# Kernel optimization log

Measured on AMD Instinct MI355X. Metric: run time of the kernel, lower is better.

## Reference

```python
import jax, jax.numpy as jnp
import numpy as np

NEG_FILL = -10000.0  # matches masked_fill_(mask, -10000.0)


def setup_inputs() -> dict:
    key0 = jax.random.key(0)
    kq, kk, kv, km = jax.random.split(key0, 4)
    B, H, S, D = 2, 16, 2048, 64
    query = jax.random.normal(kq, (B, H, S, D), dtype=jnp.float32)
    key = jax.random.normal(kk, (B, H, S, D), dtype=jnp.float32)
    value = jax.random.normal(kv, (B, H, S, D), dtype=jnp.float32)
    # key-padding mask [B, S]; True = position is masked out
    mask = jax.random.randint(km, (B, S), 0, 2).astype(jnp.bool_)
    return {"query": query, "key": key, "value": value, "mask": mask}


def reference(query, key, value, mask):
    # scaled dot-product attention: [B,H,S,D] x [B,H,S,D] -> [B,H,S,S]
    scale = 1.0 / jnp.sqrt(jnp.asarray(query.shape[-1], query.dtype))
    scores = jnp.einsum('bhqd,bhkd->bhqk', query, key) * scale
    # mask [B,S] -> broadcast over heads and query positions as [B,1,1,S]
    scores = jnp.where(mask[:, None, None, :], jnp.asarray(NEG_FILL, scores.dtype), scores)
    attn = jax.nn.softmax(scores, axis=-1)
    # dropout probs are 0 (eval-mode identity)
    out = jnp.einsum('bhqk,bhkd->bhqd', attn, value)
    return out
```

## Files before the change

kernel.cpp:

```cpp
#include <hip/hip_runtime.h>
#include <hip/hip_bf16.h>
#include <stdint.h>

namespace {

constexpr int Bb = 2;
constexpr int Hh = 16;
constexpr int Ss = 2048;
constexpr int Dd = 64;
constexpr int KT = 64;
constexpr int NT = Ss / KT;
constexpr int TILE_BYTES = KT * Dd * 2;
constexpr int BH_BYTES = NT * TILE_BYTES;
constexpr size_t KPRE_BYTES = (size_t)Bb * Hh * Ss * Dd * 2;
constexpr size_t VPRE_OFF = KPRE_BYTES;
constexpr size_t MASK_OFF = 2 * KPRE_BYTES;
constexpr size_t WS_NEED = MASK_OFF + (size_t)Bb * NT * 8;
constexpr int NIT = 16;
constexpr int IT_BYTES = 2 * TILE_BYTES;

typedef __bf16 bf16x8 __attribute__((ext_vector_type(8)));
typedef float floatx4 __attribute__((ext_vector_type(4)));

typedef __attribute__((address_space(1))) const unsigned int guint;
typedef __attribute__((address_space(3))) unsigned int luint;

__device__ __forceinline__ void g2lds16(const void* g, void* l) {
  __builtin_amdgcn_global_load_lds((guint*)g, (luint*)l, 16, 0, 0);
}

__global__ __launch_bounds__(256) void preprocess3(
    const float* __restrict__ K, const float* __restrict__ V,
    const int* __restrict__ mask, uint8_t* __restrict__ ws)
{
  const int tid = threadIdx.x;
  const int kt = blockIdx.x;
  const int bh = blockIdx.y;

  if (blockIdx.z == 0) {
    const int c = tid & 7;
#pragma unroll
    for (int half = 0; half < 2; ++half) {
      const int row = (tid >> 3) + half * 32;
      const float4* src = (const float4*)(K + ((size_t)bh * 2048 + kt * 64 + row) * 64 + c * 8);
      const float4 a = src[0], b2 = src[1];
      bf16x8 pk;
      pk[0] = (__bf16)a.x;  pk[1] = (__bf16)a.y;  pk[2] = (__bf16)a.z;  pk[3] = (__bf16)a.w;
      pk[4] = (__bf16)b2.x; pk[5] = (__bf16)b2.y; pk[6] = (__bf16)b2.z; pk[7] = (__bf16)b2.w;
      uint8_t* dst = ws + (size_t)bh * BH_BYTES + kt * TILE_BYTES + row * 128 + ((c ^ (row & 7)) << 4);
      *(bf16x8*)dst = pk;
    }
    if (bh == 0 && kt < 16) {
      const int i = kt * 256 + tid;
      const int bb = i >> 11, key = i & 2047;
      const unsigned long long bal = __ballot(mask[bb * 2048 + key] != 0);
      if ((key & 63) == 0)
        ((unsigned long long*)(ws + MASK_OFF))[bb * NT + (key >> 6)] = bal;
    }
    return;
  }

  __shared__ float Vsh[64 * 68];
#pragma unroll
  for (int i = 0; i < 4; ++i) {
    const int vt = tid + 256 * i;
    const int row = vt >> 4, c4 = vt & 15;
    const float4 v4 = *(const float4*)(V + ((size_t)bh * 2048 + kt * 64 + row) * 64 + c4 * 4);
    *(float4*)&Vsh[row * 68 + c4 * 4] = v4;
  }
  __syncthreads();
  {
    const int c16 = tid & 7;
    const int s2 = c16 & 1, q = c16 >> 1;
    const int k0 = 32 * s2 + 4 * q;
#pragma unroll
    for (int half = 0; half < 2; ++half) {
      const int d = (tid >> 3) + half * 32;
      bf16x8 pv;
#pragma unroll
      for (int j = 0; j < 4; ++j) {
        pv[j]     = (__bf16)Vsh[(k0 + j) * 68 + d];
        pv[4 + j] = (__bf16)Vsh[(k0 + 16 + j) * 68 + d];
      }
      uint8_t* dst = ws + VPRE_OFF + (size_t)bh * BH_BYTES + kt * TILE_BYTES + d * 128 + ((c16 ^ (d & 7)) << 4);
      *(bf16x8*)dst = pv;
    }
  }
}

#define NEGM (-14426.950408889634f)
#define MFMA16 __builtin_amdgcn_mfma_f32_16x16x32_bf16

__global__ __launch_bounds__(256, 2) void attn_fused7(
    const float* __restrict__ Q, const uint8_t* __restrict__ ws,
    float* __restrict__ Out)
{
  const int tid  = threadIdx.x;
  const int wave = tid >> 6;
  const int lane = tid & 63;
  const int ln   = lane & 15;
  const int quad = lane >> 4;

  const int bh   = blockIdx.x;
  const int qblk = blockIdx.y;
  const int b    = bh >> 4;

  const float* Qb = Q + (size_t)bh * Ss * Dd;
  float*       Ob = Out + (size_t)bh * Ss * Dd;
  const uint8_t* Kpre = ws + (size_t)bh * BH_BYTES;
  const uint8_t* Vpre = ws + VPRE_OFF + (size_t)bh * BH_BYTES;
  const unsigned long long* Mbits = (const unsigned long long*)(ws + MASK_OFF) + b * NT;

  __shared__ __align__(16) __bf16 Klds[2][128 * Dd];
  __shared__ __align__(16) __bf16 Vlds[2][128 * Dd];

  const int q0A = qblk * 128 + wave * 32;
  const int q0B = q0A + 16;

  const float QS = 0.125f * 1.44269504088896340736f;
  bf16x8 aqA0, aqA1, aqB0, aqB1;
  {
    const float* qpA = Qb + (size_t)(q0A + ln) * Dd + quad * 8;
    const float* qpB = Qb + (size_t)(q0B + ln) * Dd + quad * 8;
#pragma unroll
    for (int j = 0; j < 8; ++j) {
      aqA0[j] = (__bf16)(qpA[j] * QS);
      aqA1[j] = (__bf16)(qpA[32 + j] * QS);
      aqB0[j] = (__bf16)(qpB[j] * QS);
      aqB1[j] = (__bf16)(qpB[32 + j] * QS);
    }
  }

  floatx4 oA[4], oB[4];
  floatx4 laccA = (floatx4){0.f, 0.f, 0.f, 0.f};
  floatx4 laccB = (floatx4){0.f, 0.f, 0.f, 0.f};
#pragma unroll
  for (int nd = 0; nd < 4; ++nd) {
    oA[nd] = (floatx4){0.f, 0.f, 0.f, 0.f};
    oB[nd] = (floatx4){0.f, 0.f, 0.f, 0.f};
  }

  const int swz0 = (quad ^ (ln & 7)) << 4;
  const int swz1 = ((quad + 4) ^ (ln & 7)) << 4;
  const int soff = wave * 4096 + lane * 16;

#pragma unroll
  for (int i = 0; i < 4; ++i) {
    g2lds16(Kpre + soff + i * 1024, (uint8_t*)Klds[0] + soff + i * 1024);
    g2lds16(Vpre + soff + i * 1024, (uint8_t*)Vlds[0] + soff + i * 1024);
  }

  for (int kt2 = 0; kt2 < NIT; ++kt2) {
    const int cur = kt2 & 1;
    __syncthreads();

    if (kt2 + 1 < NIT) {
      const uint8_t* kg = Kpre + (kt2 + 1) * IT_BYTES;
      const uint8_t* vg = Vpre + (kt2 + 1) * IT_BYTES;
      uint8_t* kl = (uint8_t*)Klds[cur ^ 1];
      uint8_t* vl = (uint8_t*)Vlds[cur ^ 1];
#pragma unroll
      for (int i = 0; i < 4; ++i) {
        g2lds16(kg + soff + i * 1024, kl + soff + i * 1024);
        g2lds16(vg + soff + i * 1024, vl + soff + i * 1024);
      }
    }

    const unsigned long long mb0 = Mbits[2 * kt2];
    const unsigned long long mb1 = Mbits[2 * kt2 + 1];

    const uint8_t* Kb = (const uint8_t*)Klds[cur];
    const uint8_t* Vb = (const uint8_t*)Vlds[cur];

    auto loadK = [&](int sub, bf16x8& b0, bf16x8& b1) {
      const uint8_t* krow = Kb + (sub >> 2) * 8192 + ((sub & 3) * 16 + ln) * 128;
      b0 = *(const bf16x8*)(krow + swz0);
      b1 = *(const bf16x8*)(krow + swz1);
    };
    auto loadV = [&](int p, bf16x8* w) {
      const int T = p >> 1, s2 = p & 1;
#pragma unroll
      for (int nd = 0; nd < 4; ++nd) {
        const uint8_t* vrow = Vb + T * 8192 + (nd * 16 + ln) * 128;
        w[nd] = *(const bf16x8*)(vrow + (((quad * 2 + s2) ^ (ln & 7)) << 4));
      }
    };

    __builtin_amdgcn_s_setprio(1);

    bf16x8 kf0[2][2], kf1[2][2];
    bf16x8 vf[2][4];
    loadK(0, kf0[0][0], kf1[0][0]);
    loadK(1, kf0[0][1], kf1[0][1]);
    loadV(0, vf[0]);

#pragma unroll
    for (int p = 0; p < 4; ++p) {
      const int cb = p & 1, nb = cb ^ 1;

      if (p < 3) {
        loadK(2 * p + 2, kf0[nb][0], kf1[nb][0]);
        loadK(2 * p + 3, kf0[nb][1], kf1[nb][1]);
        loadV(p + 1, vf[nb]);
      }

      const unsigned long long mbx = (p & 2) ? mb1 : mb0;
      const uint32_t bits0 = (uint32_t)(mbx >> ((((2 * p) & 3) * 16) + quad * 4));
      const uint32_t bits1 = (uint32_t)(mbx >> ((((2 * p + 1) & 3) * 16) + quad * 4));
      floatx4 sA0, sA1, sB0, sB1;
#pragma unroll
      for (int r = 0; r < 4; ++r) {
        const float b0v = ((bits0 >> r) & 1) ? NEGM : 0.f;
        const float b1v = ((bits1 >> r) & 1) ? NEGM : 0.f;
        sA0[r] = b0v; sB0[r] = b0v;
        sA1[r] = b1v; sB1[r] = b1v;
      }

      sA0 = MFMA16(kf0[cb][0], aqA0, sA0, 0, 0, 0);
      sA0 = MFMA16(kf1[cb][0], aqA1, sA0, 0, 0, 0);
      sB0 = MFMA16(kf0[cb][0], aqB0, sB0, 0, 0, 0);
      sB0 = MFMA16(kf1[cb][0], aqB1, sB0, 0, 0, 0);
      sA1 = MFMA16(kf0[cb][1], aqA0, sA1, 0, 0, 0);
      sA1 = MFMA16(kf1[cb][1], aqA1, sA1, 0, 0, 0);
      sB1 = MFMA16(kf0[cb][1], aqB0, sB1, 0, 0, 0);
      sB1 = MFMA16(kf1[cb][1], aqB1, sB1, 0, 0, 0);

      bf16x8 bpA, bpB;
#pragma unroll
      for (int r = 0; r < 4; ++r) {
        const float pA0 = __builtin_amdgcn_exp2f(sA0[r]);
        const float pA1 = __builtin_amdgcn_exp2f(sA1[r]);
        const float pB0 = __builtin_amdgcn_exp2f(sB0[r]);
        const float pB1 = __builtin_amdgcn_exp2f(sB1[r]);
        laccA[r] += pA0 + pA1;
        laccB[r] += pB0 + pB1;
        bpA[r] = (__bf16)pA0; bpA[4 + r] = (__bf16)pA1;
        bpB[r] = (__bf16)pB0; bpB[4 + r] = (__bf16)pB1;
      }

#pragma unroll
      for (int nd = 0; nd < 4; ++nd) {
        oA[nd] = MFMA16(vf[cb][nd], bpA, oA[nd], 0, 0, 0);
        oB[nd] = MFMA16(vf[cb][nd], bpB, oB[nd], 0, 0, 0);
      }
    }
    __builtin_amdgcn_s_setprio(0);
  }

  float lA = (laccA[0] + laccA[1]) + (laccA[2] + laccA[3]);
  float lB = (laccB[0] + laccB[1]) + (laccB[2] + laccB[3]);
  lA += __shfl_xor(lA, 16); lA += __shfl_xor(lA, 32);
  lB += __shfl_xor(lB, 16); lB += __shfl_xor(lB, 32);
  const float iA = 1.0f / lA, iB = 1.0f / lB;
#pragma unroll
  for (int nd = 0; nd < 4; ++nd) {
    float4 wv;
    wv.x = oA[nd][0] * iA; wv.y = oA[nd][1] * iA;
    wv.z = oA[nd][2] * iA; wv.w = oA[nd][3] * iA;
    *(float4*)(Ob + (size_t)(q0A + ln) * Dd + nd * 16 + quad * 4) = wv;
    wv.x = oB[nd][0] * iB; wv.y = oB[nd][1] * iB;
    wv.z = oB[nd][2] * iB; wv.w = oB[nd][3] * iB;
    *(float4*)(Ob + (size_t)(q0B + ln) * Dd + nd * 16 + quad * 4) = wv;
  }
}

}

extern "C" void kernel_launch(void* const* d_in, const int* in_sizes, int n_in,
                              void* d_out, int out_size, void* d_ws, size_t ws_size,
                              hipStream_t stream) {
  const float* Q   = (const float*)d_in[0];
  const float* K   = (const float*)d_in[1];
  const float* V   = (const float*)d_in[2];
  const int*  mask = (const int*)d_in[3];
  float* Out = (float*)d_out;

  preprocess3<<<dim3(32, 32, 2), 256, 0, stream>>>(K, V, mask, (uint8_t*)d_ws);
  attn_fused7<<<dim3(Bb * Hh, Ss / 128), 256, 0, stream>>>(Q, (const uint8_t*)d_ws, Out);
  (void)ws_size; (void)in_sizes; (void)n_in; (void)out_size;
}
```

Before: 135.3 us.

## Split key range across two wave groups per block with LDS reduction

Result: slower. 148.1 us (+9.4%).

```diff
diff --git a/kernel.cpp b/kernel.cpp
--- a/kernel.cpp
+++ b/kernel.cpp
@@ -16,8 +16,6 @@
 constexpr size_t VPRE_OFF = KPRE_BYTES;
 constexpr size_t MASK_OFF = 2 * KPRE_BYTES;
 constexpr size_t WS_NEED = MASK_OFF + (size_t)Bb * NT * 8;
-constexpr int NIT = 16;
-constexpr int IT_BYTES = 2 * TILE_BYTES;
 
 typedef __bf16 bf16x8 __attribute__((ext_vector_type(8)));
 typedef float floatx4 __attribute__((ext_vector_type(4)));
@@ -91,12 +89,14 @@
 #define NEGM (-14426.950408889634f)
 #define MFMA16 __builtin_amdgcn_mfma_f32_16x16x32_bf16
 
-__global__ __launch_bounds__(256, 2) void attn_fused7(
+__global__ __launch_bounds__(512, 4) void attn_fused8(
     const float* __restrict__ Q, const uint8_t* __restrict__ ws,
     float* __restrict__ Out)
 {
   const int tid  = threadIdx.x;
   const int wave = tid >> 6;
+  const int kgrp = wave >> 2;
+  const int wq   = wave & 3;
   const int lane = tid & 63;
   const int ln   = lane & 15;
   const int quad = lane >> 4;
@@ -107,14 +107,15 @@
 
   const float* Qb = Q + (size_t)bh * Ss * Dd;
   float*       Ob = Out + (size_t)bh * Ss * Dd;
-  const uint8_t* Kpre = ws + (size_t)bh * BH_BYTES;
-  const uint8_t* Vpre = ws + VPRE_OFF + (size_t)bh * BH_BYTES;
-  const unsigned long long* Mbits = (const unsigned long long*)(ws + MASK_OFF) + b * NT;
-
-  __shared__ __align__(16) __bf16 Klds[2][128 * Dd];
-  __shared__ __align__(16) __bf16 Vlds[2][128 * Dd];
-
-  const int q0A = qblk * 128 + wave * 32;
+  const uint8_t* Kpre = ws + (size_t)bh * BH_BYTES + (size_t)kgrp * 16 * TILE_BYTES;
+  const uint8_t* Vpre = ws + VPRE_OFF + (size_t)bh * BH_BYTES + (size_t)kgrp * 16 * TILE_BYTES;
+  const unsigned long long* Mbits =
+      (const unsigned long long*)(ws + MASK_OFF) + b * NT + kgrp * 16;
+
+  __shared__ __align__(16) __bf16 Klds[2][2][64 * Dd];
+  __shared__ __align__(16) __bf16 Vlds[2][2][64 * Dd];
+
+  const int q0A = qblk * 128 + wq * 32;
   const int q0B = q0A + 16;
 
   const float QS = 0.125f * 1.44269504088896340736f;
@@ -142,46 +143,44 @@
 
   const int swz0 = (quad ^ (ln & 7)) << 4;
   const int swz1 = ((quad + 4) ^ (ln & 7)) << 4;
-  const int soff = wave * 4096 + lane * 16;
-
-#pragma unroll
-  for (int i = 0; i < 4; ++i) {
-    g2lds16(Kpre + soff + i * 1024, (uint8_t*)Klds[0] + soff + i * 1024);
-    g2lds16(Vpre + soff + i * 1024, (uint8_t*)Vlds[0] + soff + i * 1024);
-  }
-
-  for (int kt2 = 0; kt2 < NIT; ++kt2) {
-    const int cur = kt2 & 1;
+  const int soff = wq * 1024 + lane * 16;
+
+#pragma unroll
+  for (int i = 0; i < 2; ++i) {
+    g2lds16(Kpre + soff + i * 4096, (uint8_t*)Klds[kgrp][0] + soff + i * 4096);
+    g2lds16(Vpre + soff + i * 4096, (uint8_t*)Vlds[kgrp][0] + soff + i * 4096);
+  }
+
+  for (int it = 0; it < 16; ++it) {
+    const int cur = it & 1;
     __syncthreads();
 
-    if (kt2 + 1 < NIT) {
-      const uint8_t* kg = Kpre + (kt2 + 1) * IT_BYTES;
-      const uint8_t* vg = Vpre + (kt2 + 1) * IT_BYTES;
-      uint8_t* kl = (uint8_t*)Klds[cur ^ 1];
-      uint8_t* vl = (uint8_t*)Vlds[cur ^ 1];
-#pragma unroll
-      for (int i = 0; i < 4; ++i) {
-        g2lds16(kg + soff + i * 1024, kl + soff + i * 1024);
-        g2lds16(vg + soff + i * 1024, vl + soff + i * 1024);
-      }
-    }
-
-    const unsigned long long mb0 = Mbits[2 * kt2];
-    const unsigned long long mb1 = Mbits[2 * kt2 + 1];
-
-    const uint8_t* Kb = (const uint8_t*)Klds[cur];
-    const uint8_t* Vb = (const uint8_t*)Vlds[cur];
+    if (it + 1 < 16) {
+      const uint8_t* kg = Kpre + (it + 1) * TILE_BYTES;
+      const uint8_t* vg = Vpre + (it + 1) * TILE_BYTES;
+      uint8_t* kl = (uint8_t*)Klds[kgrp][cur ^ 1];
+      uint8_t* vl = (uint8_t*)Vlds[kgrp][cur ^ 1];
+#pragma unroll
+      for (int i = 0; i < 2; ++i) {
+        g2lds16(kg + soff + i * 4096, kl + soff + i * 4096);
+        g2lds16(vg + soff + i * 4096, vl + soff + i * 4096);
+      }
+    }
+
+    const unsigned long long mb = Mbits[it];
+
+    const uint8_t* Kb = (const uint8_t*)Klds[kgrp][cur];
+    const uint8_t* Vb = (const uint8_t*)Vlds[kgrp][cur];
 
     auto loadK = [&](int sub, bf16x8& b0, bf16x8& b1) {
-      const uint8_t* krow = Kb + (sub >> 2) * 8192 + ((sub & 3) * 16 + ln) * 128;
+      const uint8_t* krow = Kb + (sub * 16 + ln) * 128;
       b0 = *(const bf16x8*)(krow + swz0);
       b1 = *(const bf16x8*)(krow + swz1);
     };
-    auto loadV = [&](int p, bf16x8* w) {
-      const int T = p >> 1, s2 = p & 1;
+    auto loadV = [&](int s2, bf16x8* w) {
 #pragma unroll
       for (int nd = 0; nd < 4; ++nd) {
-        const uint8_t* vrow = Vb + T * 8192 + (nd * 16 + ln) * 128;
+        const uint8_t* vrow = Vb + (nd * 16 + ln) * 128;
         w[nd] = *(const bf16x8*)(vrow + (((quad * 2 + s2) ^ (ln & 7)) << 4));
       }
     };
@@ -195,18 +194,15 @@
     loadV(0, vf[0]);
 
 #pragma unroll
-    for (int p = 0; p < 4; ++p) {
-      const int cb = p & 1, nb = cb ^ 1;
-
-      if (p < 3) {
-        loadK(2 * p + 2, kf0[nb][0], kf1[nb][0]);
-        loadK(2 * p + 3, kf0[nb][1], kf1[nb][1]);
-        loadV(p + 1, vf[nb]);
-      }
-
-      const unsigned long long mbx = (p & 2) ? mb1 : mb0;
-      const uint32_t bits0 = (uint32_t)(mbx >> ((((2 * p) & 3) * 16) + quad * 4));
-      const uint32_t bits1 = (uint32_t)(mbx >> ((((2 * p + 1) & 3) * 16) + quad * 4));
+    for (int p = 0; p < 2; ++p) {
+      if (p == 0) {
+        loadK(2, kf0[1][0], kf1[1][0]);
+        loadK(3, kf0[1][1], kf1[1][1]);
+        loadV(1, vf[1]);
+      }
+
+      const uint32_t bits0 = (uint32_t)(mb >> ((2 * p) * 16 + quad * 4));
+      const uint32_t bits1 = (uint32_t)(mb >> ((2 * p + 1) * 16 + quad * 4));
       floatx4 sA0, sA1, sB0, sB1;
 #pragma unroll
       for (int r = 0; r < 4; ++r) {
@@ -216,14 +212,14 @@
         sA1[r] = b1v; sB1[r] = b1v;
       }
 
-      sA0 = MFMA16(kf0[cb][0], aqA0, sA0, 0, 0, 0);
-      sA0 = MFMA16(kf1[cb][0], aqA1, sA0, 0, 0, 0);
-      sB0 = MFMA16(kf0[cb][0], aqB0, sB0, 0, 0, 0);
-      sB0 = MFMA16(kf1[cb][0], aqB1, sB0, 0, 0, 0);
-      sA1 = MFMA16(kf0[cb][1], aqA0, sA1, 0, 0, 0);
-      sA1 = MFMA16(kf1[cb][1], aqA1, sA1, 0, 0, 0);
-      sB1 = MFMA16(kf0[cb][1], aqB0, sB1, 0, 0, 0);
-      sB1 = MFMA16(kf1[cb][1], aqB1, sB1, 0, 0, 0);
+      sA0 = MFMA16(kf0[p][0], aqA0, sA0, 0, 0, 0);
+      sA0 = MFMA16(kf1[p][0], aqA1, sA0, 0, 0, 0);
+      sB0 = MFMA16(kf0[p][0], aqB0, sB0, 0, 0, 0);
+      sB0 = MFMA16(kf1[p][0], aqB1, sB0, 0, 0, 0);
+      sA1 = MFMA16(kf0[p][1], aqA0, sA1, 0, 0, 0);
+      sA1 = MFMA16(kf1[p][1], aqA1, sA1, 0, 0, 0);
+      sB1 = MFMA16(kf0[p][1], aqB0, sB1, 0, 0, 0);
+      sB1 = MFMA16(kf1[p][1], aqB1, sB1, 0, 0, 0);
 
       bf16x8 bpA, bpB;
 #pragma unroll
@@ -240,8 +236,8 @@
 
 #pragma unroll
       for (int nd = 0; nd < 4; ++nd) {
-        oA[nd] = MFMA16(vf[cb][nd], bpA, oA[nd], 0, 0, 0);
-        oB[nd] = MFMA16(vf[cb][nd], bpB, oB[nd], 0, 0, 0);
+        oA[nd] = MFMA16(vf[p][nd], bpA, oA[nd], 0, 0, 0);
+        oB[nd] = MFMA16(vf[p][nd], bpB, oB[nd], 0, 0, 0);
       }
     }
     __builtin_amdgcn_s_setprio(0);
@@ -251,16 +247,40 @@
   float lB = (laccB[0] + laccB[1]) + (laccB[2] + laccB[3]);
   lA += __shfl_xor(lA, 16); lA += __shfl_xor(lA, 32);
   lB += __shfl_xor(lB, 16); lB += __shfl_xor(lB, 32);
-  const float iA = 1.0f / lA, iB = 1.0f / lB;
-#pragma unroll
-  for (int nd = 0; nd < 4; ++nd) {
-    float4 wv;
-    wv.x = oA[nd][0] * iA; wv.y = oA[nd][1] * iA;
-    wv.z = oA[nd][2] * iA; wv.w = oA[nd][3] * iA;
-    *(float4*)(Ob + (size_t)(q0A + ln) * Dd + nd * 16 + quad * 4) = wv;
-    wv.x = oB[nd][0] * iB; wv.y = oB[nd][1] * iB;
-    wv.z = oB[nd][2] * iB; wv.w = oB[nd][3] * iB;
-    *(float4*)(Ob + (size_t)(q0B + ln) * Dd + nd * 16 + quad * 4) = wv;
+
+  __syncthreads();
+  float* sm = (float*)&Klds[0][0][0];
+  float* sl = (float*)&Vlds[0][0][0];
+  const int mbase = (wq * 64 + lane) * 32;
+  const int sw = lane & 7;
+  if (kgrp == 1) {
+#pragma unroll
+    for (int nd = 0; nd < 4; ++nd) {
+      *(floatx4*)&sm[mbase + ((nd ^ sw) << 2)]       = oA[nd];
+      *(floatx4*)&sm[mbase + (((4 + nd) ^ sw) << 2)] = oB[nd];
+    }
+    sl[(wq * 64 + lane) * 2 + 0] = lA;
+    sl[(wq * 64 + lane) * 2 + 1] = lB;
+  }
+  __syncthreads();
+  if (kgrp == 0) {
+    lA += sl[(wq * 64 + lane) * 2 + 0];
+    lB += sl[(wq * 64 + lane) * 2 + 1];
+    const float iA = 1.0f / lA, iB = 1.0f / lB;
+#pragma unroll
+    for (int nd = 0; nd < 4; ++nd) {
+      floatx4 pA = *(const floatx4*)&sm[mbase + ((nd ^ sw) << 2)];
+      floatx4 pB = *(const floatx4*)&sm[mbase + (((4 + nd) ^ sw) << 2)];
+      pA += oA[nd];
+      pB += oB[nd];
+      float4 wv;
+      wv.x = pA[0] * iA; wv.y = pA[1] * iA;
+      wv.z = pA[2] * iA; wv.w = pA[3] * iA;
+      *(float4*)(Ob + (size_t)(q0A + ln) * Dd + nd * 16 + quad * 4) = wv;
+      wv.x = pB[0] * iB; wv.y = pB[1] * iB;
+      wv.z = pB[2] * iB; wv.w = pB[3] * iB;
+      *(float4*)(Ob + (size_t)(q0B + ln) * Dd + nd * 16 + quad * 4) = wv;
+    }
   }
 }
 
@@ -276,6 +296,6 @@
   float* Out = (float*)d_out;
 
   preprocess3<<<dim3(32, 32, 2), 256, 0, stream>>>(K, V, mask, (uint8_t*)d_ws);
-  attn_fused7<<<dim3(Bb * Hh, Ss / 128), 256, 0, stream>>>(Q, (const uint8_t*)d_ws, Out);
+  attn_fused8<<<dim3(Bb * Hh, Ss / 128), 512, 0, stream>>>(Q, (const uint8_t*)d_ws, Out);
   (void)ws_size; (void)in_sizes; (void)n_in; (void)out_size;
 }
```
